# Optimization experiments

Hardware: AMD Instinct MI355X
Metric: run time of the kernel (lower is better)

Reference implementation:

```python
import jax, jax.numpy as jnp
import numpy as np

NEG = -1.0e30  # stand-in for -inf, safe under logaddexp in fp32
DEN_SCALE = 1.0


def _ctc_forward(logp, targets, in_lens, tgt_lens):
    """Log-semiring forward (tot score) over the numerator lattice:
    CTC topology composed with the linear target FSA. logp: [B,T,C] (blank=0),
    targets: [B,U] in [1, C-1]. Returns [B] numerator log-scores."""
    B, T, C = logp.shape
    U = targets.shape[1]
    S = 2 * U + 1  # extended label sequence: blank-interleaved
    ext = jnp.zeros((B, S), dtype=jnp.int32).at[:, 1::2].set(targets.astype(jnp.int32))
    # skip transition s-2 -> s allowed only for non-blank, non-repeated labels
    skip_ok = jnp.concatenate(
        [jnp.zeros((B, 2), dtype=bool), (ext[:, 2:] != 0) & (ext[:, 2:] != ext[:, :-2])],
        axis=1,
    )
    emit0 = jnp.take_along_axis(logp[:, 0], ext, axis=1)  # [B,S]
    alpha = jnp.full((B, S), NEG, dtype=logp.dtype)
    alpha = alpha.at[:, 0].set(emit0[:, 0]).at[:, 1].set(emit0[:, 1])
    logp_t = jnp.swapaxes(logp, 0, 1)  # [T,B,C]

    def step(alpha, xs):
        t, lp = xs
        a1 = jnp.concatenate([jnp.full((B, 1), NEG, alpha.dtype), alpha[:, :-1]], axis=1)
        a2 = jnp.concatenate([jnp.full((B, 2), NEG, alpha.dtype), alpha[:, :-2]], axis=1)
        cand = jnp.logaddexp(jnp.logaddexp(alpha, a1), jnp.where(skip_ok, a2, NEG))
        new = cand + jnp.take_along_axis(lp, ext, axis=1)
        alpha = jnp.where((t < in_lens)[:, None], new, alpha)  # freeze past utterance end
        return alpha, None

    alpha, _ = jax.lax.scan(step, alpha, (jnp.arange(1, T), logp_t[1:]))
    last = (2 * tgt_lens).astype(jnp.int32)  # final states: last blank / last label
    a_last = jnp.take_along_axis(alpha, last[:, None], axis=1)[:, 0]
    a_prev = jnp.take_along_axis(alpha, (last - 1)[:, None], axis=1)[:, 0]
    return jnp.logaddexp(a_last, a_prev)


def _den_forward(logp, trans, start, in_lens):
    """Log-semiring forward over the dense denominator graph (bigram token LM):
    states = token classes, transition log-weights trans[C,C]. Returns [B]."""
    B, T, C = logp.shape
    alpha = start[None, :] + logp[:, 0]  # [B,C]
    logp_t = jnp.swapaxes(logp, 0, 1)  # [T,B,C]

    def step(alpha, xs):
        t, lp = xs
        new = jax.nn.logsumexp(alpha[:, :, None] + trans[None], axis=1) + lp
        alpha = jnp.where((t < in_lens)[:, None], new, alpha)
        return alpha, None

    alpha, _ = jax.lax.scan(step, alpha, (jnp.arange(1, T), logp_t[1:]))
    return jax.nn.logsumexp(alpha, axis=1)


def setup_inputs() -> dict:
    key = jax.random.key(0)
    ks = jax.random.split(key, 6)
    B, T, C, U = 32, 2000, 256, 200
    log_probs = jax.nn.log_softmax(jax.random.normal(ks[0], (B, T, C), dtype=jnp.float32), axis=-1)
    targets = jax.random.randint(ks[1], (B, U), 1, C)
    input_lengths = jax.random.randint(ks[2], (B,), T // 2, T + 1)
    target_lengths = jax.random.randint(ks[3], (B,), U // 2, U + 1)
    den_transitions = jax.random.normal(ks[4], (C, C), dtype=jnp.float32) * 0.1
    den_start = jax.random.normal(ks[5], (C,), dtype=jnp.float32) * 0.1
    return {
        "log_probs": log_probs,
        "targets": targets,
        "input_lengths": input_lengths,
        "target_lengths": target_lengths,
        "den_transitions": den_transitions,
        "den_start": den_start,
    }


def reference(log_probs, targets, input_lengths, target_lengths, den_transitions, den_start):
    logp = jax.nn.log_softmax(log_probs, axis=-1)  # idempotent if already normalized
    B, T, C = logp.shape
    U = targets.shape[1]
    in_lens = jnp.clip(input_lengths, 2 * U + 1, T).astype(jnp.int32)
    tgt_lens = jnp.clip(target_lengths, 1, U).astype(jnp.int32)
    tgt = jnp.clip(targets, 1, C - 1)  # blank=0 excluded from targets
    num = _ctc_forward(logp, tgt, in_lens, tgt_lens)
    den = _den_forward(logp, den_transitions, den_start, in_lens)
    tot = num - DEN_SCALE * den  # LF-MMI per-utterance objective
    valid = tot > 0.5 * NEG  # mimic get_tot_objf_and_num_frames -inf filtering
    n = jnp.maximum(jnp.sum(valid), 1)
    return -jnp.sum(jnp.where(valid, tot, 0.0)) / n
```

## Files before the change

kernel.cpp:

```cpp
#include <hip/hip_runtime.h>
#include <stdint.h>
#include <stddef.h>

#define NEGF (-1.0e30f)

typedef __attribute__((ext_vector_type(2))) _Float16 half2_t;
typedef uint32_t u32x16 __attribute__((ext_vector_type(16)));

constexpr int Bn = 32;
constexpr int Tn = 2000;
constexpr int Cn = 256;
constexpr int Un = 200;
constexpr int Sn = 2 * Un + 1;
constexpr float Kn = 4096.0f;

__device__ __forceinline__ float fdot2f(uint32_t a, uint32_t b, float c) {
  half2_t ha = __builtin_bit_cast(half2_t, a);
  half2_t hb = __builtin_bit_cast(half2_t, b);
#if __has_builtin(__builtin_amdgcn_fdot2)
  return __builtin_amdgcn_fdot2(ha, hb, c, false);
#else
  return c + (float)ha.x * (float)hb.x + (float)ha.y * (float)hb.y;
#endif
}

template <int CTRL>
__device__ __forceinline__ float dppf(float x) {
#if __has_builtin(__builtin_amdgcn_update_dpp)
  int xi = __builtin_bit_cast(int, x);
  int y = __builtin_amdgcn_update_dpp(0, xi, CTRL, 0xF, 0xF, false);
  return __builtin_bit_cast(float, y);
#else
  return x;
#endif
}
#define dpp_x1(v) dppf<0xB1>(v)
#define dpp_x2(v) dppf<0x4E>(v)
#define dpp_x7(v) dppf<0x141>(v)

__device__ __forceinline__ uint32_t packe(float a, float b) {
  half2_t h;
  h.x = (_Float16)a;
  h.y = (_Float16)b;
  return __builtin_bit_cast(uint32_t, h);
}

__device__ __forceinline__ float lse3(float a, float b, float c) {
  float m = fmaxf(fmaxf(a, b), c);
  return m + __logf(__expf(a - m) + __expf(b - m) + __expf(c - m));
}

__device__ __forceinline__ int clampi(int v, int lo, int hi) {
  return v < lo ? lo : (v > hi ? hi : v);
}

__device__ __forceinline__ void barrier_nodrain() {
  asm volatile("s_waitcnt lgkmcnt(0)" ::: "memory");
  __builtin_amdgcn_s_barrier();
  asm volatile("" ::: "memory");
}

__global__ __launch_bounds__(512)
__attribute__((amdgpu_waves_per_eu(2, 2)))
void fwd_kernel(
    const float* __restrict__ logp, const int* __restrict__ targets,
    const int* __restrict__ in_lens, const int* __restrict__ tgt_lens,
    const float* __restrict__ trans, const float* __restrict__ start,
    float* __restrict__ ws) {
  const int tid = threadIdx.x;
  const int bid = blockIdx.x;

  if (bid < Bn) {
    const int b = bid;
    const int L = clampi(in_lens[b], Sn, Tn);
    const int q = tid & 7;
    const int u = tid >> 3;
    const bool q4 = (q & 4) != 0, q2 = (q & 2) != 0, q1 = (q & 1) != 0;
    (void)q1;
    const int kk = (q4 ? 2 : 0) + (q2 ? 1 : 0);
    const int jw = u + 64 * kk;

    __shared__ __align__(16) char eaLDS[2 * 8 * 80];
    __shared__ float sred[8];

    const float* trow = trans;
#define EP(c, m) packe(__expf(trow[(32 * q + 2 * (m)) * Cn + (c)]), \
                       __expf(trow[(32 * q + 2 * (m) + 1) * Cn + (c)]))
#define MKCOL(c)                                                          \
  (u32x16){EP(c, 0),  EP(c, 1),  EP(c, 2),  EP(c, 3),  EP(c, 4),          \
           EP(c, 5),  EP(c, 6),  EP(c, 7),  EP(c, 8),  EP(c, 9),          \
           EP(c, 10), EP(c, 11), EP(c, 12), EP(c, 13), EP(c, 14), EP(c, 15)}
    u32x16 E0 = MKCOL(u + 0);
    u32x16 E1 = MKCOL(u + 64);
    u32x16 E2 = MKCOL(u + 128);
    u32x16 E3 = MKCOL(u + 192);
#undef MKCOL
#undef EP

    const float* lpb = logp + (size_t)b * Tn * Cn;
    const char* rbase0 = eaLDS + 80 * q;
    char* wptr0 = eaLDS + 80 * (2 * kk + (u >> 5)) + 2 * (u & 31);

    float G = -__logf(Kn);
    *(_Float16*)(wptr0) = (_Float16)(Kn * __expf(start[jw] + lpb[jw]));
    float lp0 = lpb[Cn + jw];
    float lp1 = lpb[(size_t)2 * Cn + jw];
    __syncthreads();

    const uint32_t ONE2 = 0x3C003C00u;

    for (int t = 1; t < L; ++t) {
      const int pr = (t - 1) & 1, pw = t & 1;
      const float lp_cur = lp0;
      lp0 = lp1;
      const int tpre = (t + 2 < L) ? t + 2 : L - 1;
      lp1 = lpb[(size_t)tpre * Cn + jw];
      const float p = __expf(lp_cur);

      const uint4* eap = (const uint4*)(rbase0 + pr * 640);
      float a0 = 0.f, a1 = 0.f, a2 = 0.f, a3 = 0.f;
      half2_t zpk = {(_Float16)0.f, (_Float16)0.f};
#define B2(x) __builtin_bit_cast(half2_t, x)
#define DOT4(idx, ev)               \
  a0 = fdot2f(E0[idx], ev, a0);     \
  a1 = fdot2f(E1[idx], ev, a1);     \
  a2 = fdot2f(E2[idx], ev, a2);     \
  a3 = fdot2f(E3[idx], ev, a3);
#define DOTQ(m4)                                                      \
  {                                                                   \
    const uint4 e4 = eap[m4];                                         \
    DOT4(4 * (m4) + 0, e4.x)                                          \
    DOT4(4 * (m4) + 1, e4.y)                                          \
    DOT4(4 * (m4) + 2, e4.z)                                          \
    DOT4(4 * (m4) + 3, e4.w)                                          \
    zpk = zpk + ((B2(e4.x) + B2(e4.y)) + (B2(e4.z) + B2(e4.w)));      \
  }
      DOTQ(0)
      DOTQ(1)
      DOTQ(2)
      DOTQ(3)
#undef DOTQ
#undef DOT4

      float zc = fdot2f(ONE2, __builtin_bit_cast(uint32_t, zpk), 0.f);
      zc += dpp_x1(zc);
      zc += dpp_x2(zc);
      zc += dpp_x7(zc);

      float g, t0, t1, w, s;
      g = q4 ? a0 : a2;  t0 = (q4 ? a2 : a0) + dpp_x7(g);
      g = q4 ? a1 : a3;  t1 = (q4 ? a3 : a1) + dpp_x7(g);
      g = q2 ? t0 : t1;  w  = (q2 ? t1 : t0) + dpp_x2(g);
      s = w + dpp_x1(w);

      const float invZ = Kn * __frcp_rn(zc);
      G -= __logf(invZ);
      *(_Float16*)(wptr0 + pw * 640) = (_Float16)(s * p * invZ);
      barrier_nodrain();
    }

    {
      const int pL = (L - 1) & 1;
      const char* fb = eaLDS + pL * 640;
      float e = 0.f;
      if (tid < 256)
        e = (float)(*(const _Float16*)(fb + 80 * (tid >> 5) + 2 * (tid & 31)));
#pragma unroll
      for (int off = 32; off >= 1; off >>= 1) e += __shfl_xor(e, off, 64);
      const int lane = tid & 63, wid = tid >> 6;
      if (lane == 0) sred[wid] = e;
      __syncthreads();
      if (tid == 0) {
        float ssum = ((sred[0] + sred[1]) + (sred[2] + sred[3])) +
                     ((sred[4] + sred[5]) + (sred[6] + sred[7]));
        ws[Bn + b] = G + __logf(ssum);
      }
    }
  } else {
    const int b = bid - Bn;
    const int L = clampi(in_lens[b], Sn, Tn);
    const int tl = clampi(tgt_lens[b], 1, Un);

    __shared__ float abuf[2][Sn + 3];
    const float* lpb = logp + (size_t)b * Tn * Cn;
    const int* tgtb = targets + b * Un;

    const int s1 = tid;
    int e1 = 0;
    bool k1 = false;
    const bool act = (s1 < Sn);
    if (act && (s1 & 1)) {
      const int uu = (s1 - 1) >> 1;
      e1 = clampi(tgtb[uu], 1, Cn - 1);
      if (uu > 0) k1 = (e1 != clampi(tgtb[uu - 1], 1, Cn - 1));
    }

    if (act) abuf[0][s1 + 2] = (s1 == 0) ? lpb[0] : (s1 == 1 ? lpb[e1] : NEGF);
    if (tid < 2) { abuf[0][tid] = NEGF; abuf[1][tid] = NEGF; }
    float pe0 = lpb[Cn + e1];
    float pe1 = lpb[(size_t)2 * Cn + e1];
    __syncthreads();

    int cur = 0;
    for (int t = 1; t < L; ++t) {
      const float em1 = pe0;
      pe0 = pe1;
      const int tpre = (t + 2 < L) ? t + 2 : L - 1;
      pe1 = lpb[(size_t)tpre * Cn + e1];
      const float* A = abuf[cur];
      float* Bv = abuf[cur ^ 1];
      if (act) {
        const float x = A[s1 + 2], y = A[s1 + 1];
        const float z = k1 ? A[s1] : NEGF;
        Bv[s1 + 2] = lse3(x, y, z) + em1;
      }
      barrier_nodrain();
      cur ^= 1;
    }
    if (tid == 0) {
      const int l = 2 * tl;
      const float x = abuf[cur][l + 2], y = abuf[cur][l + 1];
      const float m = fmaxf(x, y);
      ws[b] = m + __logf(__expf(x - m) + __expf(y - m));
    }
  }
}

__global__ void finalize_kernel(const float* __restrict__ ws,
                                float* __restrict__ out) {
  const int tid = threadIdx.x;
  float tot = 0.f, cnt = 0.f;
  if (tid < Bn) {
    const float tv = ws[tid] - ws[Bn + tid];
    const bool valid = tv > 0.5f * NEGF;
    tot = valid ? tv : 0.f;
    cnt = valid ? 1.f : 0.f;
  }
#pragma unroll
  for (int off = 32; off >= 1; off >>= 1) {
    tot += __shfl_xor(tot, off, 64);
    cnt += __shfl_xor(cnt, off, 64);
  }
  if (tid == 0) out[0] = -tot / fmaxf(cnt, 1.f);
}

extern "C" void kernel_launch(void* const* d_in, const int* in_sizes, int n_in,
                              void* d_out, int out_size, void* d_ws, size_t ws_size,
                              hipStream_t stream) {
  const float* logp = (const float*)d_in[0];
  const int* targets = (const int*)d_in[1];
  const int* in_lens = (const int*)d_in[2];
  const int* tgt_lens = (const int*)d_in[3];
  const float* trans = (const float*)d_in[4];
  const float* start = (const float*)d_in[5];
  float* ws = (float*)d_ws;
  float* out = (float*)d_out;
  (void)in_sizes; (void)n_in; (void)out_size; (void)ws_size;

  fwd_kernel<<<dim3(2 * Bn), dim3(512), 0, stream>>>(
      logp, targets, in_lens, tgt_lens, trans, start, ws);
  finalize_kernel<<<dim3(1), dim3(64), 0, stream>>>(ws, out);
}
```

Before: 1.218 ms.

## Re-split denominator matvec over 16 lanes and keep CTC alpha in registers

The denominator forward now splits each 256-wide column among 16 lanes instead of 8. Each thread holds 8 column slices of the exp-transition matrix with 8 packed half2 each, reads 32 bytes of alpha from LDS per step instead of 64, and reduces across lanes with an extra DPP stage (row_shr:15 style). The numerator CTC recursion now keeps alpha in registers and uses wavefront shuffles for the s-1 and s-2 neighbours, exchanging only wave-boundary values through a small LDS buffer each step. Both changes aim to cut per-timestep LDS traffic on the serial critical path, at the cost of more cross-lane reduction work and a different register footprint.

Result: slower. 1.258 ms (+3.3%).

```diff
diff --git a/kernel.cpp b/kernel.cpp
--- a/kernel.cpp
+++ b/kernel.cpp
@@ -5,7 +5,7 @@
 #define NEGF (-1.0e30f)
 
 typedef __attribute__((ext_vector_type(2))) _Float16 half2_t;
-typedef uint32_t u32x16 __attribute__((ext_vector_type(16)));
+typedef uint32_t u32x8 __attribute__((ext_vector_type(8)));
 
 constexpr int Bn = 32;
 constexpr int Tn = 2000;
@@ -37,12 +37,18 @@
 #define dpp_x1(v) dppf<0xB1>(v)
 #define dpp_x2(v) dppf<0x4E>(v)
 #define dpp_x7(v) dppf<0x141>(v)
+#define dpp_x15(v) dppf<0x140>(v)
 
 __device__ __forceinline__ uint32_t packe(float a, float b) {
   half2_t h;
   h.x = (_Float16)a;
   h.y = (_Float16)b;
   return __builtin_bit_cast(uint32_t, h);
+}
+
+__device__ __forceinline__ uint32_t paddh2(uint32_t a, uint32_t b) {
+  half2_t r = __builtin_bit_cast(half2_t, a) + __builtin_bit_cast(half2_t, b);
+  return __builtin_bit_cast(uint32_t, r);
 }
 
 __device__ __forceinline__ float lse3(float a, float b, float c) {
@@ -73,36 +79,42 @@
   if (bid < Bn) {
     const int b = bid;
     const int L = clampi(in_lens[b], Sn, Tn);
-    const int q = tid & 7;
-    const int u = tid >> 3;
-    const bool q4 = (q & 4) != 0, q2 = (q & 2) != 0, q1 = (q & 1) != 0;
-    (void)q1;
-    const int kk = (q4 ? 2 : 0) + (q2 ? 1 : 0);
-    const int jw = u + 64 * kk;
-
-    __shared__ __align__(16) char eaLDS[2 * 8 * 80];
+    const int q = tid & 15;
+    const int u = tid >> 4;
+    const bool b3 = (q & 8) != 0, b2 = (q & 4) != 0, b1 = (q & 2) != 0;
+    const int kk = (q >> 1);
+    const int jw = u + 32 * kk;
+
+    __shared__ __align__(16) char eaLDS[2 * 16 * 80];
     __shared__ float sred[8];
 
     const float* trow = trans;
-#define EP(c, m) packe(__expf(trow[(32 * q + 2 * (m)) * Cn + (c)]), \
-                       __expf(trow[(32 * q + 2 * (m) + 1) * Cn + (c)]))
-#define MKCOL(c)                                                          \
-  (u32x16){EP(c, 0),  EP(c, 1),  EP(c, 2),  EP(c, 3),  EP(c, 4),          \
-           EP(c, 5),  EP(c, 6),  EP(c, 7),  EP(c, 8),  EP(c, 9),          \
-           EP(c, 10), EP(c, 11), EP(c, 12), EP(c, 13), EP(c, 14), EP(c, 15)}
-    u32x16 E0 = MKCOL(u + 0);
-    u32x16 E1 = MKCOL(u + 64);
-    u32x16 E2 = MKCOL(u + 128);
-    u32x16 E3 = MKCOL(u + 192);
+#define EP(c, m) packe(__expf(trow[(16 * q + 2 * (m)) * Cn + (c)]), \
+                       __expf(trow[(16 * q + 2 * (m) + 1) * Cn + (c)]))
+#define MKCOL(c)                                                 \
+  (u32x8){EP(c, 0), EP(c, 1), EP(c, 2), EP(c, 3),                \
+          EP(c, 4), EP(c, 5), EP(c, 6), EP(c, 7)}
+    u32x8 E0 = MKCOL(u + 0);
+    u32x8 E1 = MKCOL(u + 32);
+    u32x8 E2 = MKCOL(u + 64);
+    u32x8 E3 = MKCOL(u + 96);
+    u32x8 E4 = MKCOL(u + 128);
+    u32x8 E5 = MKCOL(u + 160);
+    u32x8 E6 = MKCOL(u + 192);
+    u32x8 E7 = MKCOL(u + 224);
 #undef MKCOL
 #undef EP
 
     const float* lpb = logp + (size_t)b * Tn * Cn;
     const char* rbase0 = eaLDS + 80 * q;
-    char* wptr0 = eaLDS + 80 * (2 * kk + (u >> 5)) + 2 * (u & 31);
+    char* wptr0 = eaLDS + 80 * ((u >> 4) + 2 * kk) + 2 * (u & 15);
 
     float G = -__logf(Kn);
-    *(_Float16*)(wptr0) = (_Float16)(Kn * __expf(start[jw] + lpb[jw]));
+    if (tid < 256) {
+      const int c = tid;
+      *(_Float16*)(eaLDS + 80 * (c >> 4) + 2 * (c & 15)) =
+          (_Float16)(Kn * __expf(start[c] + lpb[c]));
+    }
     float lp0 = lpb[Cn + jw];
     float lp1 = lpb[(size_t)2 * Cn + jw];
     __syncthreads();
@@ -117,54 +129,60 @@
       lp1 = lpb[(size_t)tpre * Cn + jw];
       const float p = __expf(lp_cur);
 
-      const uint4* eap = (const uint4*)(rbase0 + pr * 640);
+      const uint4* eap = (const uint4*)(rbase0 + pr * 1280);
+      const uint4 ea0 = eap[0];
+      const uint4 ea1 = eap[1];
       float a0 = 0.f, a1 = 0.f, a2 = 0.f, a3 = 0.f;
-      half2_t zpk = {(_Float16)0.f, (_Float16)0.f};
-#define B2(x) __builtin_bit_cast(half2_t, x)
-#define DOT4(idx, ev)               \
-  a0 = fdot2f(E0[idx], ev, a0);     \
-  a1 = fdot2f(E1[idx], ev, a1);     \
-  a2 = fdot2f(E2[idx], ev, a2);     \
-  a3 = fdot2f(E3[idx], ev, a3);
-#define DOTQ(m4)                                                      \
-  {                                                                   \
-    const uint4 e4 = eap[m4];                                         \
-    DOT4(4 * (m4) + 0, e4.x)                                          \
-    DOT4(4 * (m4) + 1, e4.y)                                          \
-    DOT4(4 * (m4) + 2, e4.z)                                          \
-    DOT4(4 * (m4) + 3, e4.w)                                          \
-    zpk = zpk + ((B2(e4.x) + B2(e4.y)) + (B2(e4.z) + B2(e4.w)));      \
-  }
-      DOTQ(0)
-      DOTQ(1)
-      DOTQ(2)
-      DOTQ(3)
-#undef DOTQ
-#undef DOT4
-
-      float zc = fdot2f(ONE2, __builtin_bit_cast(uint32_t, zpk), 0.f);
+      float a4 = 0.f, a5 = 0.f, a6 = 0.f, a7 = 0.f;
+#define DOT8(idx, ev)            \
+  a0 = fdot2f(E0[idx], ev, a0);  \
+  a1 = fdot2f(E1[idx], ev, a1);  \
+  a2 = fdot2f(E2[idx], ev, a2);  \
+  a3 = fdot2f(E3[idx], ev, a3);  \
+  a4 = fdot2f(E4[idx], ev, a4);  \
+  a5 = fdot2f(E5[idx], ev, a5);  \
+  a6 = fdot2f(E6[idx], ev, a6);  \
+  a7 = fdot2f(E7[idx], ev, a7);
+      DOT8(0, ea0.x)
+      DOT8(1, ea0.y)
+      DOT8(2, ea0.z)
+      DOT8(3, ea0.w)
+      DOT8(4, ea1.x)
+      DOT8(5, ea1.y)
+      DOT8(6, ea1.z)
+      DOT8(7, ea1.w)
+#undef DOT8
+
+      uint32_t zt = paddh2(paddh2(ea0.x, ea0.y), paddh2(ea0.z, ea0.w));
+      zt = paddh2(zt, paddh2(paddh2(ea1.x, ea1.y), paddh2(ea1.z, ea1.w)));
+      float zc = fdot2f(ONE2, zt, 0.f);
       zc += dpp_x1(zc);
       zc += dpp_x2(zc);
       zc += dpp_x7(zc);
-
-      float g, t0, t1, w, s;
-      g = q4 ? a0 : a2;  t0 = (q4 ? a2 : a0) + dpp_x7(g);
-      g = q4 ? a1 : a3;  t1 = (q4 ? a3 : a1) + dpp_x7(g);
-      g = q2 ? t0 : t1;  w  = (q2 ? t1 : t0) + dpp_x2(g);
-      s = w + dpp_x1(w);
+      zc += dpp_x15(zc);
+
+      float g, r0, r1, r2, r3, w0, w1, v, s;
+      g = b3 ? a0 : a4;  r0 = (b3 ? a4 : a0) + dpp_x15(g);
+      g = b3 ? a1 : a5;  r1 = (b3 ? a5 : a1) + dpp_x15(g);
+      g = b3 ? a2 : a6;  r2 = (b3 ? a6 : a2) + dpp_x15(g);
+      g = b3 ? a3 : a7;  r3 = (b3 ? a7 : a3) + dpp_x15(g);
+      g = b2 ? r0 : r2;  w0 = (b2 ? r2 : r0) + dpp_x7(g);
+      g = b2 ? r1 : r3;  w1 = (b2 ? r3 : r1) + dpp_x7(g);
+      g = b1 ? w0 : w1;  v  = (b1 ? w1 : w0) + dpp_x2(g);
+      s = v + dpp_x1(v);
 
       const float invZ = Kn * __frcp_rn(zc);
       G -= __logf(invZ);
-      *(_Float16*)(wptr0 + pw * 640) = (_Float16)(s * p * invZ);
+      *(_Float16*)(wptr0 + pw * 1280) = (_Float16)(s * p * invZ);
       barrier_nodrain();
     }
 
     {
       const int pL = (L - 1) & 1;
-      const char* fb = eaLDS + pL * 640;
+      const char* fb = eaLDS + pL * 1280;
       float e = 0.f;
       if (tid < 256)
-        e = (float)(*(const _Float16*)(fb + 80 * (tid >> 5) + 2 * (tid & 31)));
+        e = (float)(*(const _Float16*)(fb + 80 * (tid >> 4) + 2 * (tid & 15)));
 #pragma unroll
       for (int off = 32; off >= 1; off >>= 1) e += __shfl_xor(e, off, 64);
       const int lane = tid & 63, wid = tid >> 6;
@@ -181,47 +199,59 @@
     const int L = clampi(in_lens[b], Sn, Tn);
     const int tl = clampi(tgt_lens[b], 1, Un);
 
-    __shared__ float abuf[2][Sn + 3];
+    __shared__ float bound[2][8][2];
+    __shared__ float afin[Sn];
     const float* lpb = logp + (size_t)b * Tn * Cn;
     const int* tgtb = targets + b * Un;
 
-    const int s1 = tid;
+    const int s = tid;
+    const int w = tid >> 6, lane = tid & 63;
+    const bool act = (s < Sn);
     int e1 = 0;
     bool k1 = false;
-    const bool act = (s1 < Sn);
-    if (act && (s1 & 1)) {
-      const int uu = (s1 - 1) >> 1;
+    if (act && (s & 1)) {
+      const int uu = (s - 1) >> 1;
       e1 = clampi(tgtb[uu], 1, Cn - 1);
       if (uu > 0) k1 = (e1 != clampi(tgtb[uu - 1], 1, Cn - 1));
     }
 
-    if (act) abuf[0][s1 + 2] = (s1 == 0) ? lpb[0] : (s1 == 1 ? lpb[e1] : NEGF);
-    if (tid < 2) { abuf[0][tid] = NEGF; abuf[1][tid] = NEGF; }
+    float aS = NEGF;
+    if (act) aS = (s == 0) ? lpb[0] : (s == 1 ? lpb[e1] : NEGF);
+    if (lane == 62) bound[0][w][0] = aS;
+    if (lane == 63) bound[0][w][1] = aS;
     float pe0 = lpb[Cn + e1];
     float pe1 = lpb[(size_t)2 * Cn + e1];
     __syncthreads();
 
-    int cur = 0;
     for (int t = 1; t < L; ++t) {
-      const float em1 = pe0;
+      const int pr = (t - 1) & 1, pw = t & 1;
+      const float em = pe0;
       pe0 = pe1;
       const int tpre = (t + 2 < L) ? t + 2 : L - 1;
       pe1 = lpb[(size_t)tpre * Cn + e1];
-      const float* A = abuf[cur];
-      float* Bv = abuf[cur ^ 1];
-      if (act) {
-        const float x = A[s1 + 2], y = A[s1 + 1];
-        const float z = k1 ? A[s1] : NEGF;
-        Bv[s1 + 2] = lse3(x, y, z) + em1;
+
+      float y = __shfl_up(aS, 1, 64);
+      float z = __shfl_up(aS, 2, 64);
+      if (lane == 0) {
+        y = (w > 0) ? bound[pr][w - 1][1] : NEGF;
+        z = (w > 0) ? bound[pr][w - 1][0] : NEGF;
+      } else if (lane == 1) {
+        z = (w > 0) ? bound[pr][w - 1][1] : NEGF;
       }
+      const float zm = k1 ? z : NEGF;
+      float nv = lse3(aS, y, zm) + em;
+      if (act) aS = nv;
+      if (lane == 62) bound[pw][w][0] = aS;
+      if (lane == 63) bound[pw][w][1] = aS;
       barrier_nodrain();
-      cur ^= 1;
-    }
+    }
+    if (act) afin[s] = aS;
+    __syncthreads();
     if (tid == 0) {
       const int l = 2 * tl;
-      const float x = abuf[cur][l + 2], y = abuf[cur][l + 1];
-      const float m = fmaxf(x, y);
-      ws[b] = m + __logf(__expf(x - m) + __expf(y - m));
+      const float x = afin[l], yv = afin[l - 1];
+      const float m = fmaxf(x, yv);
+      ws[b] = m + __logf(__expf(x - m) + __expf(yv - m));
     }
   }
 }
```
